# Optimization experiments

Measured on AMD Instinct MI355X. Metric: run time of the kernel, lower is better.

The kernel has to match this reference:

```python
import jax, jax.numpy as jnp
import numpy as np

SEQ, BATCH, HID, LAYERS = 512, 64, 1024, 2
SCALE = 0.02  # keep tanh out of full saturation for weight init


def setup_inputs() -> dict:
    key = jax.random.key(0)
    ks = jax.random.split(key, 6)
    return {
        "x": jax.random.normal(ks[0], (SEQ, BATCH, HID), dtype=jnp.float32),
        "h0": jax.random.normal(ks[1], (LAYERS, BATCH, HID), dtype=jnp.float32),
        "Wx": jax.random.normal(ks[2], (LAYERS, HID, HID), dtype=jnp.float32) * SCALE,
        "bx": jax.random.normal(ks[3], (LAYERS, HID), dtype=jnp.float32) * SCALE,
        "Wh": jax.random.normal(ks[4], (LAYERS, HID, HID), dtype=jnp.float32) * SCALE,
        "bh": jax.random.normal(ks[5], (LAYERS, HID), dtype=jnp.float32) * SCALE,
    }


def reference(x, h0, Wx, bx, Wh, bh):
    # x: [T, B, H]; h0: [L, B, H]; Wx/Wh: [L, H, H]; bx/bh: [L, H]
    num_layers = h0.shape[0]

    def step(h, x_t):
        # h: [L, B, H]; x_t: [B, H]
        inp = x_t
        new_h = []
        for l in range(num_layers):
            igate = inp @ Wx[l].T + bx[l]
            hgate = h[l] @ Wh[l].T + bh[l]
            h_l = jnp.tanh(igate + hgate)
            new_h.append(h_l)
            inp = h_l
        h_next = jnp.stack(new_h)
        return h_next, 10.0 * h_next[-1]

    h_n, output = jax.lax.scan(step, h0, x)
    return output, h_n
```

## Files before the change

### kernel.cpp

```cpp
#include <hip/hip_runtime.h>
#include <cstddef>
#include <cstdint>

#define HID     1024
#define BATCH   64
#define TSEQ    512
#define NB      (BATCH*HID)
#define NBLK    256
#define NITER   515
#define RSTRIDE 20


typedef __attribute__((ext_vector_type(4))) float f32x4;
typedef __attribute__((ext_vector_type(2))) float f32x2;

#define WAITV(N) do { asm volatile("s_waitcnt vmcnt(" #N ")" ::: "memory"); \
                      __builtin_amdgcn_sched_barrier(0); } while (0)

__device__ __forceinline__ f32x4 gload4(const float* p) {
  f32x4 v;
  asm volatile("global_load_dwordx4 %0, %1, off" : "=v"(v) : "v"(p) : "memory");
  return v;
}

__device__ __forceinline__ float gload1(const float* p) {
  float v;
  asm volatile("global_load_dword %0, %1, off" : "=v"(v) : "v"(p) : "memory");
  return v;
}

__device__ __forceinline__ void gstore2_coh(float* p, f32x2 v) {
  asm volatile("global_store_dwordx2 %0, %1, off sc1" :: "v"(p), "v"(v) : "memory");
}

__device__ __forceinline__ void gbar(unsigned* bar, unsigned target) {
  asm volatile("s_waitcnt vmcnt(0)" ::: "memory");
  __syncthreads();
  if (threadIdx.x == 0) {
    __hip_atomic_fetch_add(bar, 1u, __ATOMIC_RELAXED, __HIP_MEMORY_SCOPE_AGENT);
    while (__hip_atomic_load(bar, __ATOMIC_RELAXED, __HIP_MEMORY_SCOPE_AGENT) < target) {
      __builtin_amdgcn_s_sleep(1);
    }
  }
  __syncthreads();
}

__device__ __forceinline__ void load16(float (&A)[16], const float* hTb, int k0) {
#pragma unroll
  for (int j = 0; j < 16; ++j) A[j] = gload1(hTb + (size_t)(k0 + j) * 64);
}

__device__ __forceinline__ void fma16t(f32x2 (&acc)[16], const float (&h)[16], const float* Wc) {
#pragma unroll 4
  for (int c = 0; c < 16; ++c) {
    const float* w = Wc + (size_t)c * HID;
    float4 w0 = *(const float4*)(w + 0);
    float4 w1 = *(const float4*)(w + 4);
    float4 w2 = *(const float4*)(w + 8);
    float4 w3 = *(const float4*)(w + 12);
    f32x2 s = acc[c];
    s += f32x2{h[0],  h[1]}  * f32x2{w0.x, w0.y};
    s += f32x2{h[2],  h[3]}  * f32x2{w0.z, w0.w};
    s += f32x2{h[4],  h[5]}  * f32x2{w1.x, w1.y};
    s += f32x2{h[6],  h[7]}  * f32x2{w1.z, w1.w};
    s += f32x2{h[8],  h[9]}  * f32x2{w2.x, w2.y};
    s += f32x2{h[10], h[11]} * f32x2{w2.z, w2.w};
    s += f32x2{h[12], h[13]} * f32x2{w3.x, w3.y};
    s += f32x2{h[14], h[15]} * f32x2{w3.z, w3.w};
    acc[c] = s;
  }
}

__device__ __forceinline__ void dot_engine_T(const float* hTb, const float* Wb,
                                             int k0, f32x2 (&acc)[16]) {
  float A[16], B[16];
  load16(A, hTb, k0);
  load16(B, hTb, k0 + 16);
  WAITV(16); fma16t(acc, A, Wb);
  load16(A, hTb, k0 + 32);
  WAITV(16); fma16t(acc, B, Wb + 16);
  load16(B, hTb, k0 + 48);
  WAITV(16); fma16t(acc, A, Wb + 32);
  load16(A, hTb, k0 + 64);
  WAITV(16); fma16t(acc, B, Wb + 48);
  load16(B, hTb, k0 + 80);
  WAITV(16); fma16t(acc, A, Wb + 64);
  load16(A, hTb, k0 + 96);
  WAITV(16); fma16t(acc, B, Wb + 80);
  load16(B, hTb, k0 + 112);
  WAITV(16); fma16t(acc, A, Wb + 96);
  WAITV(0);  fma16t(acc, B, Wb + 112);
}

__device__ __forceinline__ void fma16x4(f32x2 (&acc)[16], const f32x4 (&h)[8], const float* Wc) {
#pragma unroll 4
  for (int c = 0; c < 16; ++c) {
    const float* w = Wc + (size_t)c * HID;
    f32x2 s = acc[c];
#pragma unroll
    for (int r = 0; r < 8; ++r) {
      float4 wv = *(const float4*)(w + r * 4);
      s += f32x2{h[r].x, h[r].y} * f32x2{wv.x, wv.y};
      s += f32x2{h[r].z, h[r].w} * f32x2{wv.z, wv.w};
    }
    acc[c] = s;
  }
}

__device__ __forceinline__ void dot_engine_x(const float* hb, const float* Wb, f32x2 (&acc)[16]) {
  f32x4 A[8], B[8];
#pragma unroll
  for (int r = 0; r < 8; ++r) A[r] = gload4(hb + r * 4);
#pragma unroll
  for (int r = 0; r < 8; ++r) B[r] = gload4(hb + 32 + r * 4);
  WAITV(8); fma16x4(acc, A, Wb);
#pragma unroll
  for (int r = 0; r < 8; ++r) A[r] = gload4(hb + 64 + r * 4);
  WAITV(8); fma16x4(acc, B, Wb + 32);
#pragma unroll
  for (int r = 0; r < 8; ++r) B[r] = gload4(hb + 96 + r * 4);
  WAITV(8); fma16x4(acc, A, Wb + 64);
  WAITV(0); fma16x4(acc, B, Wb + 96);
}

__global__ __launch_bounds__(256) void init_hT(
    const float* __restrict__ h0_init, float* __restrict__ ws,
    unsigned P, unsigned mask)
{
  const int g = blockIdx.x * 256 + threadIdx.x;
  const int l = g >> 16;
  const int r = g & 65535;
  const int k = r >> 6;
  const int b = r & 63;
  float* base = ws + (size_t)l * P * NB + (size_t)mask * NB;
  base[r] = h0_init[(size_t)l * NB + (size_t)b * HID + k];
}

__global__ __launch_bounds__(512, 2) void rnn_step(
    const float* __restrict__ x,
    float* io,
    const float* __restrict__ Wx,
    const float* __restrict__ Wh,
    const float* __restrict__ bx,
    const float* __restrict__ bh,
    float* __restrict__ ws,
    unsigned P, unsigned mask)
{
  __shared__ __align__(16) float red[8 * 64 * RSTRIDE];
  const int tid  = threadIdx.x;
  const int blk  = blockIdx.x;
  const int role = blk >> 6;
  const int c0   = (blk & 63) << 4;
  const int b    = tid & 63;
  const int kq   = __builtin_amdgcn_readfirstlane(tid >> 6);
  const int k0   = kq * 128;

  float* h0base = ws;
  float* h1base = ws + (size_t)P * NB;
  float* igbase = ws + (size_t)2 * P * NB;
  unsigned* bar = (unsigned*)(ws + (size_t)3 * P * NB);

  const float* W = (role == 3) ? Wx
                 : (role == 0) ? Wh
                 : (role == 1) ? (Wx + (size_t)HID * HID)
                 :               (Wh + (size_t)HID * HID);
  const float* Wb = W + (size_t)c0 * HID + k0;

  const int cE = tid >> 5;
  const int bE = (tid & 31) << 1;
  const size_t rbT = (size_t)(c0 + cE) * 64 + bE;

  float bsum = 0.f;
  if (role == 1)      bsum = bx[HID + c0 + cE] + bh[HID + c0 + cE];
  else if (role == 3) bsum = bx[c0 + cE]       + bh[c0 + cE];

  for (int i = 0; i < NITER; ++i) {
    if ((i & (int)mask) == 0 && i) {
      __builtin_amdgcn_fence(__ATOMIC_ACQUIRE, "agent");
    }

    bool active;
    int t;
    const float* src;
    if (role == 3)      { t = i;     active = (i <= 511);           src = x + (size_t)t * NB; }
    else if (role == 0) { t = i - 1; active = (i >= 1 && i <= 512);
                          src = h0base + (size_t)((t - 1) & (int)mask) * NB; }
    else if (role == 1) { t = i - 2; active = (i >= 2 && i <= 513);
                          src = h0base + (size_t)(t & (int)mask) * NB; }
    else                { t = i - 3; active = (i >= 3 && i <= 514);
                          src = h1base + (size_t)((t - 1) & (int)mask) * NB; }

    if (active) {
      f32x2 acc[16];
#pragma unroll
      for (int c = 0; c < 16; ++c) acc[c] = f32x2{0.f, 0.f};

      if (role == 3) dot_engine_x(src + (size_t)b * HID + k0, Wb, acc);
      else           dot_engine_T(src + b, Wb, k0, acc);

      f32x2 e = { 0.f, 0.f };
      if (role == 0)      e = *(const f32x2*)(io + (size_t)t * NB + rbT);
      else if (role == 2) e = *(const f32x2*)(igbase + (size_t)(t & (int)mask) * NB + rbT);

      float accs[16];
#pragma unroll
      for (int c = 0; c < 16; ++c) accs[c] = acc[c].x + acc[c].y;

      float* rrow = &red[(kq * 64 + b) * RSTRIDE];
      *(float4*)(rrow + 0)  = make_float4(accs[0],  accs[1],  accs[2],  accs[3]);
      *(float4*)(rrow + 4)  = make_float4(accs[4],  accs[5],  accs[6],  accs[7]);
      *(float4*)(rrow + 8)  = make_float4(accs[8],  accs[9],  accs[10], accs[11]);
      *(float4*)(rrow + 12) = make_float4(accs[12], accs[13], accs[14], accs[15]);
      __syncthreads();

      float s0 = 0.f, s1 = 0.f;
#pragma unroll
      for (int q = 0; q < 8; ++q) {
        s0 += red[(q * 64 + bE)     * RSTRIDE + cE];
        s1 += red[(q * 64 + bE + 1) * RSTRIDE + cE];
      }

      if (role == 3) {
        gstore2_coh(io + (size_t)t * NB + rbT, f32x2{ s0 + bsum, s1 + bsum });
      } else if (role == 0) {
        gstore2_coh(h0base + (size_t)(t & (int)mask) * NB + rbT,
                    f32x2{ tanhf(s0 + e.x), tanhf(s1 + e.y) });
      } else if (role == 1) {
        gstore2_coh(igbase + (size_t)(t & (int)mask) * NB + rbT,
                    f32x2{ s0 + bsum, s1 + bsum });
      } else {
        float t0 = tanhf(s0 + e.x);
        float t1 = tanhf(s1 + e.y);
        gstore2_coh(h1base + (size_t)(t & (int)mask) * NB + rbT, f32x2{ t0, t1 });
        io[(size_t)t * NB + (size_t)bE       * HID + c0 + cE] = 10.f * t0;
        io[(size_t)t * NB + (size_t)(bE + 1) * HID + c0 + cE] = 10.f * t1;
      }
    }
    gbar(bar, (unsigned)(NBLK * (i + 1)));
  }
}

__global__ __launch_bounds__(256) void finalize_hn(
    const float* __restrict__ ws, float* __restrict__ out, unsigned P, unsigned mask)
{
  const int g = blockIdx.x * 256 + threadIdx.x;
  const int l = g >> 16;
  const int rem = g & 65535;
  const int bb = rem >> 10;
  const int kk = rem & 1023;
  const float* hf = ws + ((size_t)l * P + (511u & mask)) * NB;
  out[(size_t)TSEQ * NB + g] = hf[(size_t)kk * 64 + bb];
}

extern "C" void kernel_launch(void* const* d_in, const int* in_sizes, int n_in,
                              void* d_out, int out_size, void* d_ws, size_t ws_size,
                              hipStream_t stream) {
  const float* x  = (const float*)d_in[0];
  const float* h0 = (const float*)d_in[1];
  const float* Wx = (const float*)d_in[2];
  const float* bx = (const float*)d_in[3];
  const float* Wh = (const float*)d_in[4];
  const float* bh = (const float*)d_in[5];
  float* out = (float*)d_out;
  float* ws  = (float*)d_ws;

  unsigned P = 16;
  while (P > 2 && ((size_t)3 * P * NB + 16) * sizeof(float) > ws_size) P >>= 1;
  unsigned mask = P - 1;

  hipMemsetAsync(ws + (size_t)3 * P * NB, 0, sizeof(unsigned), stream);
  init_hT<<<dim3(512), dim3(256), 0, stream>>>(h0, ws, P, mask);

  float* io = out;
  void* args[] = { &x, &io, &Wx, &Wh, &bx, &bh, &ws, &P, &mask };
  hipLaunchCooperativeKernel((const void*)rnn_step, dim3(NBLK), dim3(512),
                             args, 0, stream);

  finalize_hn<<<dim3(512), dim3(256), 0, stream>>>(ws, out, P, mask);
}
```

Measured before the change: 17.85 ms.

## Software-pipeline weight loads via explicit asm with SGPR bases and double buffering

Replaces the compiler-generated weight loads in the dot engines with inline-asm dwordx4 loads that use a scalar base per output row and a shared vector offset, double-buffered against hidden-state loads. The k loop is restructured into 4-wide sections over a rolled loop, with explicit vmcnt waits so weight and hidden-state fetches overlap the FMAs. This aims to hide weight-load latency and reduce address-computation VGPR pressure. The cost is more in-flight registers (32 f32x4 buffers), a rolled loop, and reliance on exact wait counts being correct.

New measurement: 23.22 ms. 30.1% more time.

```diff
diff --git a/kernel.cpp b/kernel.cpp
--- a/kernel.cpp
+++ b/kernel.cpp
@@ -17,17 +17,16 @@
 #define WAITV(N) do { asm volatile("s_waitcnt vmcnt(" #N ")" ::: "memory"); \
                       __builtin_amdgcn_sched_barrier(0); } while (0)
 
-__device__ __forceinline__ f32x4 gload4(const float* p) {
-  f32x4 v;
-  asm volatile("global_load_dwordx4 %0, %1, off" : "=v"(v) : "v"(p) : "memory");
-  return v;
-}
-
-__device__ __forceinline__ float gload1(const float* p) {
-  float v;
-  asm volatile("global_load_dword %0, %1, off" : "=v"(v) : "v"(p) : "memory");
-  return v;
-}
+#define WLOAD(dst, base, voff, imm) \
+  asm volatile("global_load_dwordx4 %0, %1, %2 offset:" #imm \
+               : "=v"(dst) : "v"(voff), "s"(base) : "memory")
+
+#define HLOAD1(dst, p, imm) \
+  asm volatile("global_load_dword %0, %1, off offset:" #imm \
+               : "=v"(dst) : "v"(p) : "memory")
+
+#define HLOAD4(dst, p) \
+  asm volatile("global_load_dwordx4 %0, %1, off" : "=v"(dst) : "v"(p) : "memory")
 
 __device__ __forceinline__ void gstore2_coh(float* p, f32x2 v) {
   asm volatile("global_store_dwordx2 %0, %1, off sc1" :: "v"(p), "v"(v) : "memory");
@@ -45,82 +44,87 @@
   __syncthreads();
 }
 
-__device__ __forceinline__ void load16(float (&A)[16], const float* hTb, int k0) {
-#pragma unroll
-  for (int j = 0; j < 16; ++j) A[j] = gload1(hTb + (size_t)(k0 + j) * 64);
-}
-
-__device__ __forceinline__ void fma16t(f32x2 (&acc)[16], const float (&h)[16], const float* Wc) {
-#pragma unroll 4
+__device__ __forceinline__ void fma_sec(f32x2 (&acc)[16], const f32x4 (&Wq)[16],
+                                        float h0, float h1, float h2, float h3) {
+#pragma unroll
   for (int c = 0; c < 16; ++c) {
-    const float* w = Wc + (size_t)c * HID;
-    float4 w0 = *(const float4*)(w + 0);
-    float4 w1 = *(const float4*)(w + 4);
-    float4 w2 = *(const float4*)(w + 8);
-    float4 w3 = *(const float4*)(w + 12);
     f32x2 s = acc[c];
-    s += f32x2{h[0],  h[1]}  * f32x2{w0.x, w0.y};
-    s += f32x2{h[2],  h[3]}  * f32x2{w0.z, w0.w};
-    s += f32x2{h[4],  h[5]}  * f32x2{w1.x, w1.y};
-    s += f32x2{h[6],  h[7]}  * f32x2{w1.z, w1.w};
-    s += f32x2{h[8],  h[9]}  * f32x2{w2.x, w2.y};
-    s += f32x2{h[10], h[11]} * f32x2{w2.z, w2.w};
-    s += f32x2{h[12], h[13]} * f32x2{w3.x, w3.y};
-    s += f32x2{h[14], h[15]} * f32x2{w3.z, w3.w};
+    s += f32x2{h0, h1} * f32x2{Wq[c].x, Wq[c].y};
+    s += f32x2{h2, h3} * f32x2{Wq[c].z, Wq[c].w};
     acc[c] = s;
   }
 }
 
-__device__ __forceinline__ void dot_engine_T(const float* hTb, const float* Wb,
-                                             int k0, f32x2 (&acc)[16]) {
-  float A[16], B[16];
-  load16(A, hTb, k0);
-  load16(B, hTb, k0 + 16);
-  WAITV(16); fma16t(acc, A, Wb);
-  load16(A, hTb, k0 + 32);
-  WAITV(16); fma16t(acc, B, Wb + 16);
-  load16(B, hTb, k0 + 48);
-  WAITV(16); fma16t(acc, A, Wb + 32);
-  load16(A, hTb, k0 + 64);
-  WAITV(16); fma16t(acc, B, Wb + 48);
-  load16(B, hTb, k0 + 80);
-  WAITV(16); fma16t(acc, A, Wb + 64);
-  load16(A, hTb, k0 + 96);
-  WAITV(16); fma16t(acc, B, Wb + 80);
-  load16(B, hTb, k0 + 112);
-  WAITV(16); fma16t(acc, A, Wb + 96);
-  WAITV(0);  fma16t(acc, B, Wb + 112);
-}
-
-__device__ __forceinline__ void fma16x4(f32x2 (&acc)[16], const f32x4 (&h)[8], const float* Wc) {
-#pragma unroll 4
-  for (int c = 0; c < 16; ++c) {
-    const float* w = Wc + (size_t)c * HID;
-    f32x2 s = acc[c];
-#pragma unroll
-    for (int r = 0; r < 8; ++r) {
-      float4 wv = *(const float4*)(w + r * 4);
-      s += f32x2{h[r].x, h[r].y} * f32x2{wv.x, wv.y};
-      s += f32x2{h[r].z, h[r].w} * f32x2{wv.z, wv.w};
-    }
-    acc[c] = s;
-  }
-}
-
-__device__ __forceinline__ void dot_engine_x(const float* hb, const float* Wb, f32x2 (&acc)[16]) {
-  f32x4 A[8], B[8];
-#pragma unroll
-  for (int r = 0; r < 8; ++r) A[r] = gload4(hb + r * 4);
-#pragma unroll
-  for (int r = 0; r < 8; ++r) B[r] = gload4(hb + 32 + r * 4);
-  WAITV(8); fma16x4(acc, A, Wb);
-#pragma unroll
-  for (int r = 0; r < 8; ++r) A[r] = gload4(hb + 64 + r * 4);
-  WAITV(8); fma16x4(acc, B, Wb + 32);
-#pragma unroll
-  for (int r = 0; r < 8; ++r) B[r] = gload4(hb + 96 + r * 4);
-  WAITV(8); fma16x4(acc, A, Wb + 64);
-  WAITV(0); fma16x4(acc, B, Wb + 96);
+__device__ __forceinline__ void engineT(const float* hTb, int k0,
+                                        const float* const (&Wc)[16],
+                                        f32x2 (&acc)[16]) {
+  f32x4 WA[16], WB[16];
+  float a0, a1, a2, a3, b0, b1, b2, b3;
+  const float* hp = hTb + (size_t)k0 * 64;
+  unsigned vs = 0;
+  HLOAD1(a0, hp, 0); HLOAD1(a1, hp, 256); HLOAD1(a2, hp, 512); HLOAD1(a3, hp, 768);
+#pragma unroll
+  for (int c = 0; c < 16; ++c) WLOAD(WA[c], Wc[c], vs, 0);
+  hp += 256;
+#pragma unroll 1
+  for (int g = 0; g < 15; ++g) {
+    HLOAD1(b0, hp, 0); HLOAD1(b1, hp, 256); HLOAD1(b2, hp, 512); HLOAD1(b3, hp, 768);
+#pragma unroll
+    for (int c = 0; c < 16; ++c) WLOAD(WB[c], Wc[c], vs, 16);
+    hp += 256;
+    WAITV(20);
+    fma_sec(acc, WA, a0, a1, a2, a3);
+    HLOAD1(a0, hp, 0); HLOAD1(a1, hp, 256); HLOAD1(a2, hp, 512); HLOAD1(a3, hp, 768);
+#pragma unroll
+    for (int c = 0; c < 16; ++c) WLOAD(WA[c], Wc[c], vs, 32);
+    hp += 256;
+    vs += 32;
+    WAITV(20);
+    fma_sec(acc, WB, b0, b1, b2, b3);
+  }
+  HLOAD1(b0, hp, 0); HLOAD1(b1, hp, 256); HLOAD1(b2, hp, 512); HLOAD1(b3, hp, 768);
+#pragma unroll
+  for (int c = 0; c < 16; ++c) WLOAD(WB[c], Wc[c], vs, 16);
+  WAITV(20);
+  fma_sec(acc, WA, a0, a1, a2, a3);
+  WAITV(0);
+  fma_sec(acc, WB, b0, b1, b2, b3);
+}
+
+__device__ __forceinline__ void engineX(const float* hb,
+                                        const float* const (&Wc)[16],
+                                        f32x2 (&acc)[16]) {
+  f32x4 WA[16], WB[16];
+  f32x4 ha, hbv;
+  const float* hp = hb;
+  unsigned vs = 0;
+  HLOAD4(ha, hp);
+#pragma unroll
+  for (int c = 0; c < 16; ++c) WLOAD(WA[c], Wc[c], vs, 0);
+  hp += 4;
+#pragma unroll 1
+  for (int g = 0; g < 15; ++g) {
+    HLOAD4(hbv, hp);
+#pragma unroll
+    for (int c = 0; c < 16; ++c) WLOAD(WB[c], Wc[c], vs, 16);
+    hp += 4;
+    WAITV(17);
+    fma_sec(acc, WA, ha.x, ha.y, ha.z, ha.w);
+    HLOAD4(ha, hp);
+#pragma unroll
+    for (int c = 0; c < 16; ++c) WLOAD(WA[c], Wc[c], vs, 32);
+    hp += 4;
+    vs += 32;
+    WAITV(17);
+    fma_sec(acc, WB, hbv.x, hbv.y, hbv.z, hbv.w);
+  }
+  HLOAD4(hbv, hp);
+#pragma unroll
+  for (int c = 0; c < 16; ++c) WLOAD(WB[c], Wc[c], vs, 16);
+  WAITV(17);
+  fma_sec(acc, WA, ha.x, ha.y, ha.z, ha.w);
+  WAITV(0);
+  fma_sec(acc, WB, hbv.x, hbv.y, hbv.z, hbv.w);
 }
 
 __global__ __launch_bounds__(256) void init_hT(
@@ -164,7 +168,9 @@
                  : (role == 0) ? Wh
                  : (role == 1) ? (Wx + (size_t)HID * HID)
                  :               (Wh + (size_t)HID * HID);
-  const float* Wb = W + (size_t)c0 * HID + k0;
+  const float* Wc[16];
+#pragma unroll
+  for (int c = 0; c < 16; ++c) Wc[c] = W + (size_t)(c0 + c) * HID + k0;
 
   const int cE = tid >> 5;
   const int bE = (tid & 31) << 1;
@@ -195,8 +201,8 @@
 #pragma unroll
       for (int c = 0; c < 16; ++c) acc[c] = f32x2{0.f, 0.f};
 
-      if (role == 3) dot_engine_x(src + (size_t)b * HID + k0, Wb, acc);
-      else           dot_engine_T(src + b, Wb, k0, acc);
+      if (role == 3) engineX(src + (size_t)b * HID + k0, Wc, acc);
+      else           engineT(src + b, k0, Wc, acc);
 
       f32x2 e = { 0.f, 0.f };
       if (role == 0)      e = *(const f32x2*)(io + (size_t)t * NB + rbT);
```
